# Kernel tuning notes

Hardware: AMD Instinct MI355X
Metric: run time of the kernel (lower is better)

Reference implementation:

```python
import jax, jax.numpy as jnp
import numpy as np

B, IN_DIM, L = 8, 1, 512
D_MODEL, N_LAYERS, D_STATE, HORIZON, D_CONV, EXPAND = 512, 4, 16, 96, 4, 2
D_INNER = EXPAND * D_MODEL            # 1024
DT_RANK = (D_MODEL + 15) // 16        # ceil(d_model/16) = 32
EPS = 1e-5


def setup_inputs() -> dict:
    key = jax.random.key(0)
    ks = jax.random.split(key, 10)
    s = 0.02
    f32 = jnp.float32
    return {
        "x": jax.random.normal(ks[0], (B, IN_DIM, L), f32),
        "embed_w": jax.random.normal(ks[1], (D_MODEL, IN_DIM), f32) * s,
        "embed_b": jnp.zeros((D_MODEL,), f32),
        "norm_w": jnp.ones((N_LAYERS, D_MODEL), f32),
        "in_proj_w": jax.random.normal(ks[2], (N_LAYERS, 2 * D_INNER, D_MODEL), f32) * s,
        "conv_w": jax.random.normal(ks[3], (N_LAYERS, D_INNER, D_CONV), f32) * s,
        "conv_b": jnp.zeros((N_LAYERS, D_INNER), f32),
        "x_proj_w": jax.random.normal(ks[4], (N_LAYERS, DT_RANK + 2 * D_STATE, D_INNER), f32) * s,
        "dt_w": jax.random.normal(ks[5], (N_LAYERS, D_INNER, DT_RANK), f32) * s,
        "dt_b": jax.random.uniform(ks[6], (N_LAYERS, D_INNER), f32, -4.0, -2.0),
        "A_log": jnp.log(jnp.broadcast_to(jnp.arange(1, D_STATE + 1, dtype=f32), (N_LAYERS, D_INNER, D_STATE))),
        "D": jnp.ones((N_LAYERS, D_INNER), f32),
        "out_proj_w": jax.random.normal(ks[7], (N_LAYERS, D_MODEL, D_INNER), f32) * s,
        "head_w": jax.random.normal(ks[8], (HORIZON, D_MODEL), f32) * s,
        "head_b": jnp.zeros((HORIZON,), f32),
    }


def _rmsnorm(x, w):
    return x * jax.lax.rsqrt(jnp.mean(x * x, axis=-1, keepdims=True) + EPS) * w


def _mamba_layer(x, norm_w, in_w, conv_w, conv_b, xproj_w, dt_w, dt_b, A_log, Dp, out_w):
    res = x
    h = _rmsnorm(x, norm_w)
    xz = h @ in_w.T                       # (B, L, 2*I)
    xin, z = jnp.split(xz, 2, axis=-1)
    # causal depthwise conv1d over L (left-pad d_conv-1)
    lhs = jnp.swapaxes(xin, 1, 2)         # (B, I, L)
    rhs = conv_w[:, None, :]              # (I, 1, K)
    conv = jax.lax.conv_general_dilated(
        lhs, rhs, (1,), [(D_CONV - 1, 0)],
        dimension_numbers=("NCH", "OIH", "NCH"), feature_group_count=D_INNER)
    xin = jax.nn.silu(jnp.swapaxes(conv, 1, 2) + conv_b)   # (B, L, I)
    dbc = xin @ xproj_w.T                                   # (B, L, dt_rank+2N)
    delta = jax.nn.softplus(dbc[..., :DT_RANK] @ dt_w.T + dt_b)  # (B, L, I)
    Bc = dbc[..., DT_RANK:DT_RANK + D_STATE]                # (B, L, N)
    Cc = dbc[..., DT_RANK + D_STATE:]                       # (B, L, N)
    A = -jnp.exp(A_log)                                     # (I, N)
    dA = jnp.exp(delta[..., None] * A)                      # (B, L, I, N)
    dBx = delta[..., None] * Bc[:, :, None, :] * xin[..., None]

    def step(hst, inputs):
        a, bx = inputs
        hst = a * hst + bx
        return hst, hst

    h0 = jnp.zeros((x.shape[0], D_INNER, D_STATE), x.dtype)
    _, hs = jax.lax.scan(step, h0, (jnp.swapaxes(dA, 0, 1), jnp.swapaxes(dBx, 0, 1)))
    hs = jnp.swapaxes(hs, 0, 1)                             # (B, L, I, N)
    y = jnp.einsum("blin,bln->bli", hs, Cc) + Dp * xin
    y = y * jax.nn.silu(z)
    return res + y @ out_w.T


def reference(x, embed_w, embed_b, norm_w, in_proj_w, conv_w, conv_b, x_proj_w,
              dt_w, dt_b, A_log, D, out_proj_w, head_w, head_b):
    h = jnp.swapaxes(x, 1, 2) @ embed_w.T + embed_b         # (B, L, d_model)
    for i in range(N_LAYERS):
        h = _mamba_layer(h, norm_w[i], in_proj_w[i], conv_w[i], conv_b[i],
                         x_proj_w[i], dt_w[i], dt_b[i], A_log[i], D[i], out_proj_w[i])
    return h[:, -1, :] @ head_w.T + head_b                  # (B, horizon)
```

## Files before the change

### kernel.cpp

```cpp
#include <hip/hip_runtime.h>
#include <hip/hip_bf16.h>

#define B_  8
#define L_  512
#define DM  512
#define NL  4
#define DS  16
#define HOR 96
#define DC  4
#define DI  1024
#define DTR 32

#define CHUNK 16
#define NCHK (L_/CHUNK)

typedef __bf16 bf16_t;
typedef __bf16 b8_t __attribute__((ext_vector_type(8)));
typedef __bf16 b4_t __attribute__((ext_vector_type(4)));
typedef float  f4_t __attribute__((ext_vector_type(4)));

#define LOG2E 1.44269504088896f

__device__ __forceinline__ float sigmoidf_(float x){ return 1.f/(1.f+__expf(-x)); }

__device__ __forceinline__ void async16(const bf16_t* g, bf16_t* l){
  __builtin_amdgcn_global_load_lds((const __attribute__((address_space(1))) void*)g,
                                   (__attribute__((address_space(3))) void*)l, 16, 0, 0);
}

__global__ __launch_bounds__(256) void k_prep(const float* __restrict__ p0, bf16_t* __restrict__ o0,
                                              const float* __restrict__ p1, bf16_t* __restrict__ o1,
                                              const float* __restrict__ p2, bf16_t* __restrict__ o2,
                                              const float* __restrict__ p3, bf16_t* __restrict__ o3,
                                              const float* __restrict__ x, const float* __restrict__ ew,
                                              const float* __restrict__ eb, float* __restrict__ h,
                                              const float* __restrict__ nw, bf16_t* __restrict__ hbf,
                                              float* __restrict__ sumsq){
  int blk = blockIdx.x;
  if (blk < 6528){
    int j = blk*256 + threadIdx.x;
    const int S0=1048576, S1=65536, S2=32768;
    const float* src; bf16_t* dst;
    const float* fold = nullptr;
    if (j < S0){
      src=p0; dst=o0;
      int idx4 = j<<2;
      fold = nw + ((idx4>>20)*DM) + (idx4 & (DM-1));
    }
    else if ((j-=S0) < S1){ src=p1; dst=o1; }
    else if ((j-=S1) < S2){ src=p2; dst=o2; }
    else { j-=S2; src=p3; dst=o3; }
    f4_t v = ((const f4_t*)src)[j];
    if (fold){ f4_t f = *(const f4_t*)fold; v *= f; }
    bf16_t* o = dst + (size_t)j*4;
    o[0]=(bf16_t)v[0]; o[1]=(bf16_t)v[1]; o[2]=(bf16_t)v[2]; o[3]=(bf16_t)v[3];
  } else {
    int tid = threadIdx.x;
    int j = (blk-6528)*256 + tid;
    int idx = j*4;
    int d = idx & (DM-1); int t = idx >> 9;
    float xv = x[t];
    f4_t w = *(const f4_t*)(ew + d);
    f4_t b = *(const f4_t*)(eb + d);
    f4_t v;
    #pragma unroll
    for (int c=0;c<4;c++) v[c] = xv*w[c] + b[c];
    *(f4_t*)(h + idx) = v;
    b4_t hv;
    #pragma unroll
    for (int c=0;c<4;c++) hv[c] = (bf16_t)v[c];
    *(b4_t*)(hbf + idx) = hv;
    float s = v[0]*v[0]+v[1]*v[1]+v[2]*v[2]+v[3]*v[3];
    #pragma unroll
    for (int m=32;m;m>>=1) s += __shfl_xor(s, m);
    __shared__ float red2[4];
    if ((tid&63)==0) red2[tid>>6] = s;
    __syncthreads();
    int tb = (blk-6528)*2;
    if (tid==0)   sumsq[tb]   = red2[0]+red2[1];
    if (tid==128) sumsq[tb+1] = red2[2]+red2[3];
  }
}

__global__ __launch_bounds__(256) void k_g128(const bf16_t* __restrict__ A, int lda,
                                              const bf16_t* __restrict__ W, int ldw,
                                              int K, bf16_t* __restrict__ Cbf, int ldc,
                                              const float* __restrict__ sumsq){
  __shared__ bf16_t As[4*128*32];
  __shared__ bf16_t Ws[4*128*32];
  int tid = threadIdx.x;
  int m0 = blockIdx.y*128, n0 = blockIdx.x*128;
  int wave = tid>>6, lane = tid&63;
  int wm = (wave>>1)*64, wn = (wave&1)*64;
  int lr = lane&15, q = lane>>4;
  int rs = tid>>2, cs = (tid&3)*8;
  f4_t acc[4][4] = {};
  for (int k0=0;k0<K;k0+=128){
    #pragma unroll
    for (int p=0;p<4;p++){
      #pragma unroll
      for (int s=0;s<2;s++){
        int row = s*64 + rs;
        async16(A + (size_t)(m0+row)*lda + k0 + p*32 + cs, As + p*4096 + s*2048 + tid*8);
        async16(W + (size_t)(n0+row)*ldw + k0 + p*32 + cs, Ws + p*4096 + s*2048 + tid*8);
      }
    }
    __syncthreads();
    #pragma unroll
    for (int p=0;p<4;p++){
      b8_t a[4], b[4];
      #pragma unroll
      for (int i=0;i<4;i++) a[i] = *(const b8_t*)(As + p*4096 + (wm+i*16+lr)*32 + q*8);
      #pragma unroll
      for (int j=0;j<4;j++) b[j] = *(const b8_t*)(Ws + p*4096 + (wn+j*16+lr)*32 + q*8);
      #pragma unroll
      for (int i=0;i<4;i++)
        #pragma unroll
        for (int j=0;j<4;j++)
          acc[i][j] = __builtin_amdgcn_mfma_f32_16x16x32_bf16(a[i], b[j], acc[i][j], 0,0,0);
    }
    __syncthreads();
  }
  #pragma unroll
  for (int i=0;i<4;i++){
    int rb = m0 + wm + i*16 + q*4;
    f4_t sc;
    #pragma unroll
    for (int r=0;r<4;r++) sc[r] = rsqrtf(sumsq[rb+r]*(1.f/DM) + 1e-5f);
    #pragma unroll
    for (int j=0;j<4;j++){
      int col = n0 + wn + j*16 + lr;
      #pragma unroll
      for (int r=0;r<4;r++)
        Cbf[(size_t)(rb+r)*ldc + col] = (bf16_t)(acc[i][j][r]*sc[r]);
    }
  }
}

__global__ __launch_bounds__(256) void k_gout(const bf16_t* __restrict__ A,
                                              const bf16_t* __restrict__ W,
                                              float* __restrict__ C,
                                              bf16_t* __restrict__ hbf,
                                              float* __restrict__ sumsq){
  __shared__ __align__(16) char sm[65536];
  bf16_t* As = (bf16_t*)sm;
  bf16_t* Ws = (bf16_t*)(sm + 32768);
  float*  red = (float*)sm;
  int tid = threadIdx.x;
  int m0 = blockIdx.y*64, n0 = blockIdx.x*64;
  int wave = tid>>6, lane = tid&63;
  int lr = lane&15, q = lane>>4;
  int e0 = tid*8, r0 = e0>>5, c0 = e0&31;
  f4_t acc[4][4] = {};
  for (int k0=0;k0<DI;k0+=256){
    #pragma unroll
    for (int p=0;p<8;p++){
      async16(A + (size_t)(m0+r0)*DI + k0 + p*32 + c0, As + p*2048 + e0);
      async16(W + (size_t)(n0+r0)*DI + k0 + p*32 + c0, Ws + p*2048 + e0);
    }
    __syncthreads();
    #pragma unroll
    for (int s=0;s<2;s++){
      const bf16_t* Ap = As + (2*wave+s)*2048;
      const bf16_t* Wp = Ws + (2*wave+s)*2048;
      b8_t a[4], b[4];
      #pragma unroll
      for (int i=0;i<4;i++) a[i] = *(const b8_t*)(Ap + (i*16+lr)*32 + q*8);
      #pragma unroll
      for (int j=0;j<4;j++) b[j] = *(const b8_t*)(Wp + (j*16+lr)*32 + q*8);
      #pragma unroll
      for (int i=0;i<4;i++)
        #pragma unroll
        for (int j=0;j<4;j++)
          acc[i][j] = __builtin_amdgcn_mfma_f32_16x16x32_bf16(a[i], b[j], acc[i][j], 0,0,0);
    }
    __syncthreads();
  }
  #pragma unroll
  for (int i=0;i<4;i++)
  #pragma unroll
  for (int j=0;j<4;j++)
  #pragma unroll
  for (int r=0;r<4;r++){
    int rl = i*16 + q*4 + r;
    int t4 = ((rl ^ (rl>>2)) & 3) << 2;
    int c4 = j*4 + (lr>>2);
    red[wave*4096 + rl*64 + ((c4 ^ t4)<<2) + (lr&3)] = acc[i][j][r];
  }
  __syncthreads();
  #pragma unroll
  for (int g=0;g<4;g++){
    int row = g*16 + (tid>>4);
    int t4 = ((row ^ (row>>2)) & 3) << 2;
    int fo = row*64 + (((tid&15) ^ t4) << 2);
    f4_t v = *(const f4_t*)(red + fo);
    v += *(const f4_t*)(red + 4096 + fo);
    v += *(const f4_t*)(red + 8192 + fo);
    v += *(const f4_t*)(red + 12288 + fo);
    size_t off = (size_t)(m0+row)*DM + n0 + (tid&15)*4;
    f4_t c = *(const f4_t*)(C + off);
    c += v;
    *(f4_t*)(C + off) = c;
    b4_t hv;
    #pragma unroll
    for (int k=0;k<4;k++) hv[k] = (bf16_t)c[k];
    *(b4_t*)(hbf + off) = hv;
    float s2 = c[0]*c[0]+c[1]*c[1]+c[2]*c[2]+c[3]*c[3];
    s2 += __shfl_xor(s2,1); s2 += __shfl_xor(s2,2);
    s2 += __shfl_xor(s2,4); s2 += __shfl_xor(s2,8);
    if ((tid&15)==0) atomicAdd(sumsq + m0 + row, s2);
  }
}

__global__ __launch_bounds__(256) void k_dbc(const bf16_t* __restrict__ xzbf, const float* __restrict__ cw,
                                             const float* __restrict__ cb, const bf16_t* __restrict__ wxp,
                                             float* __restrict__ part, bf16_t* __restrict__ xinbf){
  __shared__ bf16_t As[4*64*32];
  __shared__ bf16_t Ws[4*64*32];
  int tid = threadIdx.x;
  int m0 = blockIdx.x*64;
  int z = blockIdx.y;
  int kbase = z*128;
  int wave = tid>>6, lane = tid&63;
  int wm = (wave>>1)*32, wn = (wave&1)*32;
  int lr = lane&15, q = lane>>4;
  int e0 = tid*8, r0 = e0>>5, c0 = e0&31;
  int gt = m0 + r0;
  int l  = gt & (L_-1);
  f4_t acc[2][2] = {};
  #pragma unroll
  for (int p=0;p<4;p++){
    int ch = kbase + p*32 + c0;
    float cv[8];
    #pragma unroll
    for (int c=0;c<8;c++) cv[c] = cb[ch+c];
    #pragma unroll
    for (int k=0;k<DC;k++){
      if (l + k - (DC-1) >= 0){
        b8_t xv = *(const b8_t*)(xzbf + (size_t)(gt + k - (DC-1))*(2*DI) + ch);
        #pragma unroll
        for (int c=0;c<8;c++) cv[c] += (float)xv[c] * cw[(ch+c)*DC + k];
      }
    }
    b8_t av;
    #pragma unroll
    for (int c=0;c<8;c++){ float s = cv[c]*sigmoidf_(cv[c]); av[c] = (bf16_t)s; }
    *(b8_t*)(As + p*2048 + e0) = av;
    *(b8_t*)(xinbf + (size_t)gt*DI + ch) = av;
    async16(wxp + (size_t)r0*DI + kbase + p*32 + c0, Ws + p*2048 + e0);
  }
  __syncthreads();
  #pragma unroll
  for (int p=0;p<4;p++){
    b8_t a[2], b[2];
    #pragma unroll
    for (int i=0;i<2;i++) a[i] = *(const b8_t*)(As + p*2048 + (wm+i*16+lr)*32 + q*8);
    #pragma unroll
    for (int j=0;j<2;j++) b[j] = *(const b8_t*)(Ws + p*2048 + (wn+j*16+lr)*32 + q*8);
    #pragma unroll
    for (int i=0;i<2;i++)
      #pragma unroll
      for (int j=0;j<2;j++)
        acc[i][j] = __builtin_amdgcn_mfma_f32_16x16x32_bf16(a[i], b[j], acc[i][j], 0,0,0);
  }
  float* P = part + (size_t)z*(B_*L_*64);
  #pragma unroll
  for (int i=0;i<2;i++)
  #pragma unroll
  for (int j=0;j<2;j++){
    int col = wn + j*16 + lr;
    int rb  = m0 + wm + i*16 + q*4;
    #pragma unroll
    for (int r=0;r<4;r++) P[(size_t)(rb+r)*64 + col] = acc[i][j][r];
  }
}

__global__ __launch_bounds__(256) void k_dt(const float* __restrict__ part, const bf16_t* __restrict__ wdt,
                                            const float* __restrict__ dtb, float* __restrict__ dbc,
                                            bf16_t* __restrict__ delta){
  __shared__ bf16_t As[64*32];
  __shared__ bf16_t Ws[64*32];
  int tid = threadIdx.x;
  int m0 = blockIdx.y*64, n0 = blockIdx.x*64;
  const size_t S = (size_t)B_*L_*64;
  int r0 = tid>>2, c0 = (tid&3)*8;
  int gt = m0 + r0;
  size_t base = (size_t)gt*64 + c0;
  f4_t s0 = *(const f4_t*)(part + base);
  f4_t s1 = *(const f4_t*)(part + base + 4);
  #pragma unroll
  for (int z=1;z<8;z++){
    s0 += *(const f4_t*)(part + z*S + base);
    s1 += *(const f4_t*)(part + z*S + base + 4);
  }
  b8_t av;
  #pragma unroll
  for (int c=0;c<4;c++){ av[c] = (bf16_t)s0[c]; av[4+c] = (bf16_t)s1[c]; }
  *(b8_t*)(As + tid*8) = av;
  if (n0 == 0){
    f4_t t0 = *(const f4_t*)(part + base + 32);
    f4_t t1 = *(const f4_t*)(part + base + 36);
    #pragma unroll
    for (int z=1;z<8;z++){
      t0 += *(const f4_t*)(part + z*S + base + 32);
      t1 += *(const f4_t*)(part + z*S + base + 36);
    }
    *(f4_t*)(dbc + base + 32) = t0;
    *(f4_t*)(dbc + base + 36) = t1;
  }
  async16(wdt + (size_t)(n0+r0)*DTR + c0, Ws + tid*8);
  __syncthreads();
  int wave = tid>>6, lane = tid&63;
  int wm = (wave>>1)*32, wn = (wave&1)*32;
  int lr = lane&15, q = lane>>4;
  b8_t a[2], b[2];
  #pragma unroll
  for (int i=0;i<2;i++) a[i] = *(const b8_t*)(As + (wm+i*16+lr)*32 + q*8);
  #pragma unroll
  for (int j=0;j<2;j++) b[j] = *(const b8_t*)(Ws + (wn+j*16+lr)*32 + q*8);
  f4_t acc[2][2] = {};
  #pragma unroll
  for (int i=0;i<2;i++)
    #pragma unroll
    for (int j=0;j<2;j++)
      acc[i][j] = __builtin_amdgcn_mfma_f32_16x16x32_bf16(a[i], b[j], acc[i][j], 0,0,0);
  #pragma unroll
  for (int i=0;i<2;i++)
  #pragma unroll
  for (int j=0;j<2;j++){
    int col = n0 + wn + j*16 + lr;
    int rb  = m0 + wm + i*16 + q*4;
    #pragma unroll
    for (int r=0;r<4;r++){
      float xv = acc[i][j][r] + dtb[col];
      float v = (xv>20.f)?xv:log1pf(__expf(xv));
      delta[(size_t)(rb+r)*DI + col] = (bf16_t)v;
    }
  }
}

__global__ __launch_bounds__(256) void k_scan_p1(const bf16_t* __restrict__ delta, const bf16_t* __restrict__ xin,
                                                 const float* __restrict__ dbc, const float* __restrict__ Alog,
                                                 bf16_t* __restrict__ hend, bf16_t* __restrict__ aprod){
  __shared__ bf16_t des[CHUNK][256];
  __shared__ bf16_t xs[CHUNK][256];
  __shared__ float Bs[CHUNK][DS];
  int tid = threadIdx.x;
  int blk = blockIdx.x;
  int chgrp = blk & 3;
  int chunk = (blk>>2) & (NCHK-1);
  int b = blk >> 7;
  int ch0 = chgrp<<8;
  int ch = ch0 + tid;
  int t0 = (b<<9) + chunk*CHUNK;
  #pragma unroll
  for (int idx=tid; idx<CHUNK*32; idx+=256){
    int row = idx>>5, c = (idx&31)*8;
    *(b8_t*)(&des[row][c]) = *(const b8_t*)(delta + (size_t)(t0+row)*DI + ch0 + c);
    *(b8_t*)(&xs[row][c])  = *(const b8_t*)(xin   + (size_t)(t0+row)*DI + ch0 + c);
  }
  {
    int ll = tid>>4, n = tid&15;
    Bs[ll][n] = dbc[(t0+ll)*64 + DTR + n];
  }
  __syncthreads();
  float An2[DS], h[DS];
  const f4_t* Ap = (const f4_t*)(Alog + ch*DS);
  #pragma unroll
  for (int v=0;v<4;v++){
    f4_t a4 = Ap[v];
    #pragma unroll
    for (int k=0;k<4;k++){ An2[v*4+k] = -__expf(a4[k])*LOG2E; h[v*4+k]=0.f; }
  }
  float sde = 0.f;
  #pragma unroll
  for (int l=0;l<CHUNK;l++){
    float de = (float)des[l][tid];
    float xv = (float)xs[l][tid];
    float dx = de*xv;
    sde += de;
    #pragma unroll
    for (int n=0;n<DS;n++){
      float dA = exp2f(de*An2[n]);
      h[n] = dA*h[n] + dx*Bs[l][n];
    }
  }
  size_t base = ((size_t)chunk*(B_*DI) + (b<<10) + ch)*DS;
  b8_t hv[2], av[2];
  #pragma unroll
  for (int v=0;v<2;v++)
    #pragma unroll
    for (int k=0;k<8;k++){
      hv[v][k] = (bf16_t)h[v*8+k];
      av[v][k] = (bf16_t)exp2f(An2[v*8+k]*sde);
    }
  ((b8_t*)(hend + base))[0] = hv[0]; ((b8_t*)(hend + base))[1] = hv[1];
  ((b8_t*)(aprod + base))[0] = av[0]; ((b8_t*)(aprod + base))[1] = av[1];
}

__global__ __launch_bounds__(256) void k_scan_p2(const bf16_t* __restrict__ hend, bf16_t* __restrict__ ap_hin,
                                                 float* __restrict__ sumsq){
  if (blockIdx.x < 16) sumsq[(blockIdx.x<<8) | threadIdx.x] = 0.f;
  int g = blockIdx.x*256 + threadIdx.x;
  float h = 0.f;
  for (int c=0;c<NCHK;c++){
    size_t off = (size_t)c*(B_*DI*DS) + g;
    float a = (float)ap_hin[off];
    float e = (float)hend[off];
    ap_hin[off] = (bf16_t)h;
    h = a*h + e;
  }
}

__global__ __launch_bounds__(256) void k_scan_p3(const bf16_t* __restrict__ delta, const bf16_t* __restrict__ xz,
                                                 const bf16_t* __restrict__ xin,
                                                 const float* __restrict__ dbc, const float* __restrict__ Alog,
                                                 const bf16_t* __restrict__ hin, const float* __restrict__ Dp,
                                                 bf16_t* __restrict__ ybf){
  __shared__ bf16_t des[CHUNK][256];
  __shared__ bf16_t xs[CHUNK][256];
  __shared__ bf16_t zs[CHUNK][256];
  __shared__ float Bs[CHUNK][DS];
  __shared__ float Cs[CHUNK][DS];
  int tid = threadIdx.x;
  int blk = blockIdx.x;
  int chgrp = blk & 3;
  int chunk = (blk>>2) & (NCHK-1);
  int b = blk >> 7;
  int ch0 = chgrp<<8;
  int ch = ch0 + tid;
  int t0 = (b<<9) + chunk*CHUNK;
  #pragma unroll
  for (int idx=tid; idx<CHUNK*32; idx+=256){
    int row = idx>>5, c = (idx&31)*8;
    *(b8_t*)(&des[row][c]) = *(const b8_t*)(delta + (size_t)(t0+row)*DI + ch0 + c);
    *(b8_t*)(&xs[row][c])  = *(const b8_t*)(xin   + (size_t)(t0+row)*DI + ch0 + c);
    *(b8_t*)(&zs[row][c])  = *(const b8_t*)(xz + (size_t)(t0+row)*(2*DI) + DI + ch0 + c);
  }
  {
    int ll = tid>>4, n = tid&15;
    Bs[ll][n] = dbc[(t0+ll)*64 + DTR + n];
    Cs[ll][n] = dbc[(t0+ll)*64 + DTR + DS + n];
  }
  __syncthreads();
  float An2[DS], h[DS];
  const f4_t* Ap = (const f4_t*)(Alog + ch*DS);
  size_t base = ((size_t)chunk*(B_*DI) + (b<<10) + ch)*DS;
  b8_t h0 = ((const b8_t*)(hin + base))[0];
  b8_t h1 = ((const b8_t*)(hin + base))[1];
  #pragma unroll
  for (int v=0;v<4;v++){
    f4_t a4 = Ap[v];
    #pragma unroll
    for (int k=0;k<4;k++){
      An2[v*4+k] = -__expf(a4[k])*LOG2E;
      int idx = v*4+k;
      h[idx] = (idx<8) ? (float)h0[idx] : (float)h1[idx-8];
    }
  }
  float Dv = Dp[ch];
  bf16_t* yp = ybf + (size_t)t0*DI + ch;
  #pragma unroll
  for (int l=0;l<CHUNK;l++){
    float de = (float)des[l][tid];
    float zv = (float)zs[l][tid];
    float xv = (float)xs[l][tid];
    float dx = de*xv;
    float y = 0.f;
    #pragma unroll
    for (int n=0;n<DS;n++){
      float dA = exp2f(de*An2[n]);
      h[n] = dA*h[n] + dx*Bs[l][n];
      y += h[n]*Cs[l][n];
    }
    y = (y + Dv*xv) * (zv * sigmoidf_(zv));
    yp[(size_t)l*DI] = (bf16_t)y;
  }
}

__global__ __launch_bounds__(256) void k_head(const float* __restrict__ h, const float* __restrict__ hw,
                                              const float* __restrict__ hb, float* __restrict__ out){
  int wave = threadIdx.x>>6, lane = threadIdx.x&63;
  int gw = blockIdx.x*4 + wave;
  int b = gw / HOR, hh = gw % HOR;
  const float* hp = h + ((size_t)b*L_ + (L_-1))*DM;
  const float* wp = hw + (size_t)hh*DM;
  float s = 0.f;
  #pragma unroll
  for (int k=0;k<DM;k+=64) s += hp[k+lane]*wp[k+lane];
  #pragma unroll
  for (int m=32;m;m>>=1) s += __shfl_xor(s, m);
  if (lane==0) out[gw] = s + hb[hh];
}

extern "C" void kernel_launch(void* const* d_in, const int* in_sizes, int n_in,
                              void* d_out, int out_size, void* d_ws, size_t ws_size,
                              hipStream_t stream){
  const float* x    = (const float*)d_in[0];
  const float* ew   = (const float*)d_in[1];
  const float* eb   = (const float*)d_in[2];
  const float* nw   = (const float*)d_in[3];
  const float* ipw  = (const float*)d_in[4];
  const float* cw   = (const float*)d_in[5];
  const float* cb   = (const float*)d_in[6];
  const float* xpw  = (const float*)d_in[7];
  const float* dtw  = (const float*)d_in[8];
  const float* dtb  = (const float*)d_in[9];
  const float* alog = (const float*)d_in[10];
  const float* Dp   = (const float*)d_in[11];
  const float* opw  = (const float*)d_in[12];
  const float* hw   = (const float*)d_in[13];
  const float* hb   = (const float*)d_in[14];
  float* out = (float*)d_out;

  char* ws = (char*)d_ws;
  size_t o = 0;
  float*  h      = (float*)(ws + o);  o += (size_t)8<<20;
  bf16_t* hbf    = (bf16_t*)(ws + o); o += (size_t)4<<20;
  bf16_t* xzbf   = (bf16_t*)(ws + o); o += (size_t)16<<20;
  bf16_t* xinbf  = (bf16_t*)(ws + o); o += (size_t)8<<20;
  bf16_t* delta  = (bf16_t*)(ws + o); o += (size_t)8<<20;
  bf16_t* ybf    = (bf16_t*)(ws + o); o += (size_t)8<<20;
  float*  dbc    = (float*)(ws + o);  o += (size_t)1<<20;
  float*  dbcp   = (float*)(ws + o);  o += (size_t)8<<20;
  bf16_t* w_in   = (bf16_t*)(ws + o); o += (size_t)8<<20;
  bf16_t* w_out  = (bf16_t*)(ws + o); o += (size_t)4<<20;
  bf16_t* w_xp   = (bf16_t*)(ws + o); o += (size_t)1<<19;
  bf16_t* w_dt   = (bf16_t*)(ws + o); o += (size_t)1<<18;
  bf16_t* hend   = (bf16_t*)(ws + o); o += (size_t)8<<20;
  bf16_t* aphin  = (bf16_t*)(ws + o); o += (size_t)8<<20;
  float*  sumsq  = (float*)(ws + o);  o += (size_t)1<<16;

  k_prep<<<8576,256,0,stream>>>(ipw, w_in, xpw, w_xp, dtw, w_dt, opw, w_out,
                                x, ew, eb, h, nw, hbf, sumsq);

  for (int i=0;i<NL;i++){
    k_g128<<<dim3(2*DI/128, B_*L_/128),256,0,stream>>>(
        hbf, DM, w_in + (size_t)i*2*DI*DM, DM, DM, xzbf, 2*DI, sumsq);
    k_dbc<<<dim3(B_*L_/64, 8),256,0,stream>>>(xzbf, cw + i*DI*DC, cb + i*DI,
                                              w_xp + (size_t)i*64*DI, dbcp, xinbf);
    k_dt<<<dim3(DI/64, B_*L_/64),256,0,stream>>>(dbcp, w_dt + (size_t)i*DI*DTR,
                                                 dtb + i*DI, dbc, delta);
    k_scan_p1<<<B_*NCHK*4,256,0,stream>>>(delta, xinbf, dbc, alog + i*DI*DS, hend, aphin);
    k_scan_p2<<<(B_*DI*DS)/256,256,0,stream>>>(hend, aphin, sumsq);
    k_scan_p3<<<B_*NCHK*4,256,0,stream>>>(delta, xzbf, xinbf, dbc, alog + i*DI*DS,
                                          aphin, Dp + i*DI, ybf);
    k_gout<<<dim3(DM/64, B_*L_/64),256,0,stream>>>(ybf, w_out + (size_t)i*DM*DI, h, hbf, sumsq);
  }
  k_head<<<(B_*HOR)/4,256,0,stream>>>(h, hw, hb, out);
}
```

Before: 602.2 us.

## Double-buffer async LDS staging in in_proj and out_proj GEMMs

Both the in_proj GEMM (k_g128) and the out_proj GEMM (k_gout) now use two LDS buffers with smaller K-steps. The next tile is prefetched asynchronously while MFMAs run on the current one, using s_waitcnt vmcnt with raw barriers and raised wave priority around the MFMA block. This is meant to hide global-load latency that the old load-all-then-sync loop exposed. K is now hardcoded to 512 in k_g128. The partial vmcnt counts assume a fixed number of outstanding loads, which is fragile if the compiler reorders memory ops.

```diff
diff --git a/kernel.cpp b/kernel.cpp
--- a/kernel.cpp
+++ b/kernel.cpp
@@ -84,42 +84,56 @@
 
 __global__ __launch_bounds__(256) void k_g128(const bf16_t* __restrict__ A, int lda,
                                               const bf16_t* __restrict__ W, int ldw,
-                                              int K, bf16_t* __restrict__ Cbf, int ldc,
+                                              bf16_t* __restrict__ Cbf, int ldc,
                                               const float* __restrict__ sumsq){
-  __shared__ bf16_t As[4*128*32];
-  __shared__ bf16_t Ws[4*128*32];
+  __shared__ __align__(16) bf16_t As[2][2*4096];
+  __shared__ __align__(16) bf16_t Ws[2][2*4096];
   int tid = threadIdx.x;
   int m0 = blockIdx.y*128, n0 = blockIdx.x*128;
   int wave = tid>>6, lane = tid&63;
   int wm = (wave>>1)*64, wn = (wave&1)*64;
   int lr = lane&15, q = lane>>4;
-  int rs = tid>>2, cs = (tid&3)*8;
+  int srow = tid>>2;
+  int scol = (tid&3)*8;
   f4_t acc[4][4] = {};
-  for (int k0=0;k0<K;k0+=128){
-    #pragma unroll
-    for (int p=0;p<4;p++){
-      #pragma unroll
-      for (int s=0;s<2;s++){
-        int row = s*64 + rs;
-        async16(A + (size_t)(m0+row)*lda + k0 + p*32 + cs, As + p*4096 + s*2048 + tid*8);
-        async16(W + (size_t)(n0+row)*ldw + k0 + p*32 + cs, Ws + p*4096 + s*2048 + tid*8);
-      }
-    }
-    __syncthreads();
-    #pragma unroll
-    for (int p=0;p<4;p++){
+  auto stage = [&](int buf, int k0){
+    #pragma unroll
+    for (int s=0;s<4;s++){
+      int hh = s>>1, p = s&1;
+      int row = hh*64 + srow;
+      async16(A + (size_t)(m0+row)*lda + k0 + p*32 + scol,
+              &As[buf][p*4096 + row*32 + scol]);
+      async16(W + (size_t)(n0+row)*ldw + k0 + p*32 + scol,
+              &Ws[buf][p*4096 + row*32 + scol]);
+    }
+  };
+  stage(0, 0);
+  #pragma unroll
+  for (int it=0; it<8; ++it){
+    if (it<7){
+      stage((it+1)&1, (it+1)*64);
+      asm volatile("s_waitcnt vmcnt(8)" ::: "memory");
+    } else {
+      asm volatile("s_waitcnt vmcnt(0)" ::: "memory");
+    }
+    __builtin_amdgcn_s_barrier();
+    int buf = it&1;
+    __builtin_amdgcn_s_setprio(1);
+    #pragma unroll
+    for (int p=0;p<2;p++){
       b8_t a[4], b[4];
       #pragma unroll
-      for (int i=0;i<4;i++) a[i] = *(const b8_t*)(As + p*4096 + (wm+i*16+lr)*32 + q*8);
+      for (int i=0;i<4;i++) a[i] = *(const b8_t*)(&As[buf][p*4096 + (wm+i*16+lr)*32 + q*8]);
       #pragma unroll
-      for (int j=0;j<4;j++) b[j] = *(const b8_t*)(Ws + p*4096 + (wn+j*16+lr)*32 + q*8);
+      for (int j=0;j<4;j++) b[j] = *(const b8_t*)(&Ws[buf][p*4096 + (wn+j*16+lr)*32 + q*8]);
       #pragma unroll
       for (int i=0;i<4;i++)
         #pragma unroll
         for (int j=0;j<4;j++)
           acc[i][j] = __builtin_amdgcn_mfma_f32_16x16x32_bf16(a[i], b[j], acc[i][j], 0,0,0);
     }
-    __syncthreads();
+    __builtin_amdgcn_s_setprio(0);
+    __builtin_amdgcn_s_barrier();
   }
   #pragma unroll
   for (int i=0;i<4;i++){
@@ -150,31 +164,42 @@
   int m0 = blockIdx.y*64, n0 = blockIdx.x*64;
   int wave = tid>>6, lane = tid&63;
   int lr = lane&15, q = lane>>4;
-  int e0 = tid*8, r0 = e0>>5, c0 = e0&31;
   f4_t acc[4][4] = {};
-  for (int k0=0;k0<DI;k0+=256){
-    #pragma unroll
-    for (int p=0;p<8;p++){
-      async16(A + (size_t)(m0+r0)*DI + k0 + p*32 + c0, As + p*2048 + e0);
-      async16(W + (size_t)(n0+r0)*DI + k0 + p*32 + c0, Ws + p*2048 + e0);
-    }
-    __syncthreads();
-    #pragma unroll
-    for (int s=0;s<2;s++){
-      const bf16_t* Ap = As + (2*wave+s)*2048;
-      const bf16_t* Wp = Ws + (2*wave+s)*2048;
-      b8_t a[4], b[4];
+  auto stage = [&](int buf, int k0){
+    #pragma unroll
+    for (int p=0;p<4;p++){
+      async16(A + (size_t)(m0+(tid>>2))*DI + k0 + p*32 + (tid&3)*8,
+              As + buf*8192 + p*2048 + tid*8);
+      async16(W + (size_t)(n0+(tid>>2))*DI + k0 + p*32 + (tid&3)*8,
+              Ws + buf*8192 + p*2048 + tid*8);
+    }
+  };
+  stage(0, 0);
+  #pragma unroll
+  for (int it=0; it<8; ++it){
+    if (it<7){
+      stage((it+1)&1, (it+1)*128);
+      asm volatile("s_waitcnt vmcnt(8)" ::: "memory");
+    } else {
+      asm volatile("s_waitcnt vmcnt(0)" ::: "memory");
+    }
+    __builtin_amdgcn_s_barrier();
+    int buf = it&1;
+    const bf16_t* Ap = As + buf*8192 + wave*2048;
+    const bf16_t* Wp = Ws + buf*8192 + wave*2048;
+    b8_t a[4], b[4];
+    #pragma unroll
+    for (int i=0;i<4;i++) a[i] = *(const b8_t*)(Ap + (i*16+lr)*32 + q*8);
+    #pragma unroll
+    for (int j=0;j<4;j++) b[j] = *(const b8_t*)(Wp + (j*16+lr)*32 + q*8);
+    __builtin_amdgcn_s_setprio(1);
+    #pragma unroll
+    for (int i=0;i<4;i++)
       #pragma unroll
-      for (int i=0;i<4;i++) a[i] = *(const b8_t*)(Ap + (i*16+lr)*32 + q*8);
-      #pragma unroll
-      for (int j=0;j<4;j++) b[j] = *(const b8_t*)(Wp + (j*16+lr)*32 + q*8);
-      #pragma unroll
-      for (int i=0;i<4;i++)
-        #pragma unroll
-        for (int j=0;j<4;j++)
-          acc[i][j] = __builtin_amdgcn_mfma_f32_16x16x32_bf16(a[i], b[j], acc[i][j], 0,0,0);
-    }
-    __syncthreads();
+      for (int j=0;j<4;j++)
+        acc[i][j] = __builtin_amdgcn_mfma_f32_16x16x32_bf16(a[i], b[j], acc[i][j], 0,0,0);
+    __builtin_amdgcn_s_setprio(0);
+    __builtin_amdgcn_s_barrier();
   }
   #pragma unroll
   for (int i=0;i<4;i++)
@@ -536,7 +561,7 @@
 
   for (int i=0;i<NL;i++){
     k_g128<<<dim3(2*DI/128, B_*L_/128),256,0,stream>>>(
-        hbf, DM, w_in + (size_t)i*2*DI*DM, DM, DM, xzbf, 2*DI, sumsq);
+        hbf, DM, w_in + (size_t)i*2*DI*DM, DM, xzbf, 2*DI, sumsq);
     k_dbc<<<dim3(B_*L_/64, 8),256,0,stream>>>(xzbf, cw + i*DI*DC, cb + i*DI,
                                               w_xp + (size_t)i*64*DI, dbcp, xinbf);
     k_dt<<<dim3(DI/64, B_*L_/64),256,0,stream>>>(dbcp, w_dt + (size_t)i*DI*DTR,
```

Result: no change. 599.4 us (-0.5%).
